# Kernel tuning notes

Hardware: AMD Instinct MI355X
Metric: run time of the kernel (lower is better)

## Reference

```python
import jax, jax.numpy as jnp
import numpy as np

B, L, D_IN, D_MODEL, D_OUT, N_LAYERS, N2 = 16, 2048, 512, 512, 512, 4, 32
Q_STEP = 1.0 / 64.0
LN_EPS = 1e-5


def setup_inputs() -> dict:
    key = jax.random.key(0)
    ks = jax.random.split(key, 12)
    H = D_MODEL
    x = jax.random.normal(ks[0], (B, D_IN, L), jnp.float32)
    # sigma-delta dense encoder / decoder weights (ANN-equivalent: dense + ReLU)
    W_enc = jax.random.normal(ks[1], (H, D_IN), jnp.float32) * (1.0 / np.sqrt(D_IN))
    W_dec = jax.random.normal(ks[2], (D_OUT, H), jnp.float32) * (1.0 / np.sqrt(H))
    # S4D kernel params, stacked over layers. S4D-Lin init.
    log_dt = (jax.random.uniform(ks[3], (N_LAYERS, H), jnp.float32)
              * (np.log(0.1) - np.log(0.001)) + np.log(0.001))
    log_A_real = jnp.full((N_LAYERS, H, N2), np.log(0.5), jnp.float32)
    A_imag = jnp.tile((np.pi * jnp.arange(N2, dtype=jnp.float32))[None, None, :],
                      (N_LAYERS, H, 1))
    C_re = jax.random.normal(ks[4], (N_LAYERS, H, N2), jnp.float32) * (0.5 ** 0.5)
    C_im = jax.random.normal(ks[5], (N_LAYERS, H, N2), jnp.float32) * (0.5 ** 0.5)
    D = jax.random.normal(ks[6], (N_LAYERS, H), jnp.float32)
    # output linear of each S4D block: 1x1 conv H -> 2H followed by GLU
    W_out = jax.random.normal(ks[7], (N_LAYERS, 2 * H, H), jnp.float32) * (1.0 / np.sqrt(H))
    b_out = jnp.zeros((N_LAYERS, 2 * H), jnp.float32)
    ln_g = jnp.ones((N_LAYERS, H), jnp.float32)
    ln_b = jnp.zeros((N_LAYERS, H), jnp.float32)
    return {"x": x, "W_enc": W_enc, "W_dec": W_dec, "log_dt": log_dt,
            "log_A_real": log_A_real, "A_imag": A_imag, "C_re": C_re,
            "C_im": C_im, "D": D, "W_out": W_out, "b_out": b_out,
            "ln_g": ln_g, "ln_b": ln_b}


def _quantize_ste(x, step):
    q = jnp.round(x / step) * step
    return x + jax.lax.stop_gradient(q - x)


def reference(x, W_enc, W_dec, log_dt, log_A_real, A_imag, C_re, C_im, D,
              W_out, b_out, ln_g, ln_b):
    # x: (B, d_input, L) channel-time layout (slayer convention)
    xq = _quantize_ste(x, Q_STEP)
    h = jax.nn.relu(jnp.einsum('bct,dc->bdt', xq, W_enc))  # encoder (B,H,L)
    Lx = h.shape[-1]
    t = jnp.arange(Lx)
    for i in range(N_LAYERS):
        # ---- S4D kernel (ZOH-style discretization) ----
        dt = jnp.exp(log_dt[i])[:, None]                 # (H,1)
        A = -jnp.exp(log_A_real[i]) + 1j * A_imag[i]     # (H,N)
        dtA = dt * A                                     # (H,N)
        Cc = (C_re[i] + 1j * C_im[i]) * jnp.expm1(dtA) / A
        vand = jnp.exp(dtA[:, :, None] * t)              # (H,N,L)
        K = 2.0 * jnp.einsum('hn,hnl->hl', Cc, vand).real  # (H,L)
        # ---- FFT convolution ----
        k_f = jnp.fft.rfft(K, n=2 * Lx)                  # (H, L+1)
        u_f = jnp.fft.rfft(h, n=2 * Lx)                  # (B,H,L+1)
        y = jnp.fft.irfft(u_f * k_f[None], n=2 * Lx)[..., :Lx]
        y = y + D[i][:, None] * h                        # skip connection
        y = jax.nn.gelu(y, approximate=False)
        # output linear: 1x1 conv H->2H + GLU over channel dim
        z = jnp.einsum('bht,dh->bdt', y, W_out[i]) + b_out[i][None, :, None]
        z = z[:, :D_MODEL] * jax.nn.sigmoid(z[:, D_MODEL:])
        # residual + post-norm (LayerNorm over channel dim)
        h = z + h
        mu = h.mean(axis=1, keepdims=True)
        var = h.var(axis=1, keepdims=True)
        h = (h - mu) / jnp.sqrt(var + LN_EPS) * ln_g[i][:, None] + ln_b[i][:, None]
    out = jax.nn.relu(jnp.einsum('bht,dh->bdt', h, W_dec))  # decoder (B,d_out,L)
    return out
```

## Files before the change

### kernel.cpp

```cpp
#include <hip/hip_runtime.h>
#include <cstdint>
#include <cstddef>

typedef __attribute__((ext_vector_type(8))) short short8;
typedef __attribute__((ext_vector_type(8))) _Float16 half8;
typedef __attribute__((ext_vector_type(4))) float floatx4;
typedef __attribute__((ext_vector_type(4))) int intx4;
typedef __attribute__((ext_vector_type(4))) unsigned short ushort4v;

__device__ __forceinline__ unsigned short f2h(float f) {
    union { _Float16 h; unsigned short u; } v;
    v.h = (_Float16)f;
    return v.u;
}
__device__ __forceinline__ float h2f(unsigned short u) {
    union { unsigned short u; _Float16 h; } v;
    v.u = u;
    return (float)v.h;
}
__device__ __forceinline__ float relu_keepnan(float v) {
    return v > 0.f ? v : (v == v ? 0.f : v);
}

__global__ __launch_bounds__(256) void k_cvt(
    const float* __restrict__ src, unsigned short* __restrict__ dst, int n) {
    int i = blockIdx.x * 256 + threadIdx.x;
    if (i < n) dst[i] = f2h(src[i]);
}

__global__ __launch_bounds__(256) void k_precompute(
    const float* __restrict__ ldt, const float* __restrict__ lar,
    const float* __restrict__ aim, const float* __restrict__ cre,
    const float* __restrict__ cim, float4* __restrict__ lwc,
    float2* __restrict__ wt) {
    int idx = blockIdx.x * 256 + threadIdx.x;
    int i = idx >> 14;
    int h = (idx >> 5) & 511;
    int n = idx & 31;
    float dt = expf(ldt[i * 512 + h]);
    float Are = -expf(lar[idx]);
    float Aim = aim[idx];
    float dre = dt * Are, dim = dt * Aim;
    float e = expf(dre);
    float wre = e * cosf(dim);
    float wim = e * sinf(dim);
    float emr = wre - 1.f, emi = wim;
    float inv = 1.f / (Are * Are + Aim * Aim);
    float fr = (emr * Are + emi * Aim) * inv;
    float fi = (emi * Are - emr * Aim) * inv;
    float cr = cre[idx], ci = cim[idx];
    float4 o;
    o.x = wre; o.y = wim;
    o.z = 2.f * (cr * fr - ci * fi);
    o.w = 2.f * (cr * fi + ci * fr);
    int oidx = (i * 32 + n) * 512 + h;
    lwc[oidx] = o;
    float ar = wre, ai = wim;
#pragma unroll
    for (int k = 0; k < 7; ++k) {
        float nr = ar * ar - ai * ai;
        float ni = 2.f * ar * ai;
        ar = nr; ai = ni;
    }
    wt[oidx] = make_float2(ar, ai);
}

__global__ __launch_bounds__(256) void k_quant_transpose(
    const float* __restrict__ x, unsigned short* __restrict__ xq, int b0) {
    __shared__ unsigned short tile[64][65];
    const int bg = b0 + blockIdx.z, bl = blockIdx.z;
    const int c0 = blockIdx.y * 64, t0 = blockIdx.x * 64;
    const int tid = threadIdx.x;
#pragma unroll
    for (int it = 0; it < 16; ++it) {
        int idx = it * 256 + tid;
        int r = idx >> 6, cc = idx & 63;
        float f = x[(size_t)(bg * 512 + c0 + r) * 2048 + t0 + cc];
        float q = rintf(f * 64.f) * 0.015625f;
        tile[r][cc] = f2h(q);
    }
    __syncthreads();
#pragma unroll
    for (int it = 0; it < 16; ++it) {
        int idx = it * 256 + tid;
        int r = idx >> 6, cc = idx & 63;
        xq[(size_t)(bl * 2048 + t0 + r) * 512 + c0 + cc] = tile[cc][r];
    }
}

__global__ __launch_bounds__(64) void k_build_wa(
    const float4* __restrict__ lwc, unsigned short* __restrict__ WA, int layer) {
    __shared__ unsigned short Ws[64 * 136];
    const int h = blockIdx.x, tid = threadIdx.x;
    if (tid < 32) {
        float4 v = lwc[((size_t)layer * 32 + tid) * 512 + h];
        float pr = 1.f, pi = 0.f;
        for (int m = 0; m < 128; ++m) {
            Ws[(2 * tid) * 136 + (127 - m)] = f2h(pr);
            Ws[(2 * tid + 1) * 136 + (127 - m)] = f2h(pi);
            float nr = pr * v.x - pi * v.y;
            float ni = pr * v.y + pi * v.x;
            pr = nr; pi = ni;
        }
    }
    __syncthreads();
#pragma unroll
    for (int it = 0; it < 16; ++it) {
        int idx = it * 64 + tid;
        int r = idx >> 4, c8 = idx & 15;
        *(intx4*)(WA + (size_t)h * 8192 + r * 128 + c8 * 8) =
            *(const intx4*)(Ws + r * 136 + c8 * 8);
    }
}

__global__ __launch_bounds__(256) void k_build_T(
    const float4* __restrict__ lwc, const float* __restrict__ Dp,
    unsigned short* __restrict__ TT, int layer) {
    __shared__ float Kvs[128];
    __shared__ unsigned short Mxs[128 * 64];
    __shared__ float wr_s[32], wi_s[32], cr_s[32], ci_s[32];
    const int h = blockIdx.x, tid = threadIdx.x;
    if (tid < 32) {
        float4 v = lwc[((size_t)layer * 32 + tid) * 512 + h];
        wr_s[tid] = v.x; wi_s[tid] = v.y; cr_s[tid] = v.z; ci_s[tid] = v.w;
    }
    __syncthreads();
    if (tid < 32) {
        const int n = tid;
        float wre = wr_s[n], wim = wi_s[n];
        float ar = cr_s[n], ai = ci_s[n];
        for (int m = 0; m <= 128; ++m) {
            if (m < 128) {
                float s = ar;
#pragma unroll
                for (int d = 16; d >= 1; d >>= 1) s += __shfl_xor(s, d, 64);
                if (n == 0) Kvs[m] = s;
            }
            if (m >= 1) {
                Mxs[(m - 1) * 64 + 2 * n] = f2h(ar);
                Mxs[(m - 1) * 64 + 2 * n + 1] = f2h(-ai);
            }
            float nr = ar * wre - ai * wim;
            float ni = ar * wim + ai * wre;
            ar = nr; ai = ni;
        }
    }
    __syncthreads();
    const float Dh = Dp[layer * 512 + h];
#pragma unroll
    for (int it = 0; it < 12; ++it) {
        int idx = it * 256 + tid;
        int t = idx / 24, c8 = idx % 24;
        short8 pack;
#pragma unroll
        for (int q = 0; q < 8; ++q) {
            int k = c8 * 8 + q;
            unsigned short us;
            if (k < 128) {
                float val = (k <= t) ? (Kvs[t - k] + (k == t ? Dh : 0.f)) : 0.f;
                us = f2h(val);
            } else {
                us = Mxs[t * 64 + (k - 128)];
            }
            pack[q] = (short)us;
        }
        *(short8*)(TT + (size_t)h * 24576 + t * 192 + c8 * 8) = pack;
    }
}

template <int MODE>
__global__ __launch_bounds__(256, 3) void k_gemm(
    const unsigned short* __restrict__ A, const unsigned short* __restrict__ Bm,
    float* __restrict__ of32, unsigned short* __restrict__ o16,
    unsigned short* __restrict__ ut, int J, int b0) {
    __shared__ __align__(16) unsigned short lds[2 * 128 * 72];
    unsigned short* Al = lds;
    unsigned short* Bl = lds + 128 * 72;
    const int tid = threadIdx.x;
    const int m0 = blockIdx.y * 128;
    const int j0 = blockIdx.x * 128;
    const int sub = tid & 7;
    const int row = tid >> 3;
    const unsigned short* Ag = A + (size_t)(m0 + row) * 512 + sub * 8;
    const unsigned short* Bg = Bm + (size_t)(j0 + row) * 512 + sub * 8;
    intx4 ra[4], rb[4];
#pragma unroll
    for (int i = 0; i < 4; ++i) {
        ra[i] = *(const intx4*)(Ag + (size_t)i * 32 * 512);
        rb[i] = *(const intx4*)(Bg + (size_t)i * 32 * 512);
    }
    const int lane = tid & 63;
    const int w = tid >> 6;
    const int wm = w & 1, wn = w >> 1;
    const int l15 = lane & 15, quad = lane >> 4;
    floatx4 acc[4][4] = {};
    for (int kt = 0; kt < 8; ++kt) {
#pragma unroll
        for (int i = 0; i < 4; ++i) {
            *(intx4*)(Al + (row + 32 * i) * 72 + sub * 8) = ra[i];
            *(intx4*)(Bl + (row + 32 * i) * 72 + sub * 8) = rb[i];
        }
        __syncthreads();
        if (kt < 7) {
#pragma unroll
            for (int i = 0; i < 4; ++i) {
                ra[i] = *(const intx4*)(Ag + (size_t)i * 32 * 512 + (kt + 1) * 64);
                rb[i] = *(const intx4*)(Bg + (size_t)i * 32 * 512 + (kt + 1) * 64);
            }
        }
#pragma unroll
        for (int ks = 0; ks < 2; ++ks) {
            half8 af[4], bfr[4];
#pragma unroll
            for (int mt = 0; mt < 4; ++mt)
                af[mt] = *(const half8*)(Al + (wm * 64 + mt * 16 + l15) * 72 + ks * 32 + quad * 8);
#pragma unroll
            for (int nt = 0; nt < 4; ++nt)
                bfr[nt] = *(const half8*)(Bl + (wn * 64 + nt * 16 + l15) * 72 + ks * 32 + quad * 8);
#pragma unroll
            for (int mt = 0; mt < 4; ++mt)
#pragma unroll
                for (int nt = 0; nt < 4; ++nt)
                    acc[mt][nt] = __builtin_amdgcn_mfma_f32_16x16x32_f16(
                        af[mt], bfr[nt], acc[mt][nt], 0, 0, 0);
        }
        __syncthreads();
    }
#pragma unroll
    for (int mt = 0; mt < 4; ++mt) {
#pragma unroll
        for (int nt = 0; nt < 4; ++nt) {
            const int dl = wm * 64 + mt * 16 + quad * 4;
            const int jl = wn * 64 + nt * 16 + l15;
            floatx4 v = acc[mt][nt];
#pragma unroll
            for (int r = 0; r < 4; ++r) v[r] = relu_keepnan(v[r]);
            if (MODE == 0) {
                ushort4v hv;
#pragma unroll
                for (int r = 0; r < 4; ++r) hv[r] = f2h(v[r]);
                *(ushort4v*)(o16 + (size_t)(j0 + jl) * 512 + m0 + dl) = hv;
#pragma unroll
                for (int r = 0; r < 4; ++r) lds[(dl + r) * 136 + jl] = hv[r];
            } else {
                const int j = j0 + jl;
                const int bl = j >> 11, t = j & 2047;
#pragma unroll
                for (int r = 0; r < 4; ++r)
                    of32[((size_t)((b0 + bl) * 512 + m0 + dl + r)) * 2048 + t] = v[r];
            }
        }
    }
    if (MODE == 0) {
        __syncthreads();
        const int drow = tid >> 1, hh = tid & 1;
        const unsigned short* srcp = lds + drow * 136 + hh * 64;
        unsigned short* dstp = ut + (size_t)(m0 + drow) * J + j0 + hh * 64;
#pragma unroll
        for (int q = 0; q < 8; ++q)
            *(intx4*)(dstp + q * 8) = *(const intx4*)(srcp + q * 8);
    }
}

__global__ __launch_bounds__(256, 4) void k_stateA_comb(
    const unsigned short* __restrict__ WA, const unsigned short* __restrict__ ut,
    const float2* __restrict__ wt, unsigned short* __restrict__ S0,
    int layer, int J, int Rtot) {
    __shared__ __align__(16) char smem[64 * 131 * 4];
    unsigned short* Aw = (unsigned short*)smem;
    unsigned short* Bw = (unsigned short*)(smem + 64 * 72 * 2);
    float* Ps = (float*)smem;
    const int tid = threadIdx.x;
    const int h = blockIdx.y;
    const int r0 = blockIdx.x * 128;
    const int sub = tid & 7, row = tid >> 3;
    const unsigned short* Ag = WA + (size_t)h * 8192 + row * 128 + sub * 8;
    const unsigned short* Bg = ut + (size_t)h * J + (size_t)(r0 + row) * 128 + sub * 8;
    intx4 ra[2], rb[4];
    ra[0] = *(const intx4*)(Ag);
    ra[1] = *(const intx4*)(Ag + 32 * 128);
#pragma unroll
    for (int i = 0; i < 4; ++i) rb[i] = *(const intx4*)(Bg + i * 32 * 128);
    const int lane = tid & 63, w = tid >> 6;
    const int wm = w & 1, wn = w >> 1;
    const int l15 = lane & 15, quad = lane >> 4;
    floatx4 acc[2][4] = {};
    for (int kt = 0; kt < 2; ++kt) {
        *(intx4*)(Aw + row * 72 + sub * 8) = ra[0];
        *(intx4*)(Aw + (row + 32) * 72 + sub * 8) = ra[1];
#pragma unroll
        for (int i = 0; i < 4; ++i)
            *(intx4*)(Bw + (row + 32 * i) * 72 + sub * 8) = rb[i];
        __syncthreads();
        if (kt == 0) {
            ra[0] = *(const intx4*)(Ag + 64);
            ra[1] = *(const intx4*)(Ag + 32 * 128 + 64);
#pragma unroll
            for (int i = 0; i < 4; ++i) rb[i] = *(const intx4*)(Bg + i * 32 * 128 + 64);
        }
#pragma unroll
        for (int ks = 0; ks < 2; ++ks) {
            half8 af[2], bfr[4];
#pragma unroll
            for (int mt = 0; mt < 2; ++mt)
                af[mt] = *(const half8*)(Aw + (wm * 32 + mt * 16 + l15) * 72 + ks * 32 + quad * 8);
#pragma unroll
            for (int nt = 0; nt < 4; ++nt)
                bfr[nt] = *(const half8*)(Bw + (wn * 64 + nt * 16 + l15) * 72 + ks * 32 + quad * 8);
#pragma unroll
            for (int mt = 0; mt < 2; ++mt)
#pragma unroll
                for (int nt = 0; nt < 4; ++nt)
                    acc[mt][nt] = __builtin_amdgcn_mfma_f32_16x16x32_f16(
                        af[mt], bfr[nt], acc[mt][nt], 0, 0, 0);
        }
        __syncthreads();
    }
#pragma unroll
    for (int mt = 0; mt < 2; ++mt)
#pragma unroll
        for (int nt = 0; nt < 4; ++nt)
#pragma unroll
            for (int r = 0; r < 4; ++r)
                Ps[(wm * 32 + mt * 16 + quad * 4 + r) * 131 +
                   wn * 64 + nt * 16 + l15] = acc[mt][nt][r];
    __syncthreads();
    const int n = tid & 31, bl = tid >> 5;
    const float2 wv = wt[((size_t)layer * 32 + n) * 512 + h];
    unsigned int* S0w = (unsigned int*)(S0 + ((size_t)h * Rtot + r0 + bl * 16) * 64) + n;
    float ar = 0.f, ai = 0.f;
#pragma unroll
    for (int g = 0; g < 16; ++g) {
        S0w[g * 32] = (unsigned int)f2h(ar) | ((unsigned int)f2h(ai) << 16);
        float pr = Ps[(2 * n) * 131 + bl * 16 + g];
        float pi = Ps[(2 * n + 1) * 131 + bl * 16 + g];
        float nr = fmaf(wv.x, ar, fmaf(-wv.y, ai, pr));
        float ni = fmaf(wv.x, ai, fmaf(wv.y, ar, pi));
        ar = nr; ai = ni;
    }
}

__global__ __launch_bounds__(256, 3) void k_applyB(
    const unsigned short* __restrict__ TT, const unsigned short* __restrict__ ut,
    const unsigned short* __restrict__ S0, unsigned short* __restrict__ vt,
    int J, int Rtot) {
    __shared__ __align__(16) unsigned short lds[2 * 128 * 72];
    unsigned short* Al = lds;
    unsigned short* Bl = lds + 128 * 72;
    const int tid = threadIdx.x;
    const int h = blockIdx.y;
    const int r0 = blockIdx.x * 128;
    const int sub = tid & 7, row = tid >> 3;
    const unsigned short* Ag = TT + (size_t)h * 24576 + row * 192 + sub * 8;
    const unsigned short* Bu = ut + (size_t)h * J + (size_t)(r0 + row) * 128 + sub * 8;
    const unsigned short* Bs = S0 + ((size_t)h * Rtot + r0 + row) * 64 + sub * 8;
    intx4 ra[4], rb[4];
#pragma unroll
    for (int i = 0; i < 4; ++i) {
        ra[i] = *(const intx4*)(Ag + i * 32 * 192);
        rb[i] = *(const intx4*)(Bu + i * 32 * 128);
    }
    const int lane = tid & 63, w = tid >> 6;
    const int wm = w & 1, wn = w >> 1;
    const int l15 = lane & 15, quad = lane >> 4;
    floatx4 acc[4][4] = {};
    for (int kt = 0; kt < 3; ++kt) {
#pragma unroll
        for (int i = 0; i < 4; ++i) {
            *(intx4*)(Al + (row + 32 * i) * 72 + sub * 8) = ra[i];
            *(intx4*)(Bl + (row + 32 * i) * 72 + sub * 8) = rb[i];
        }
        __syncthreads();
        if (kt == 0) {
#pragma unroll
            for (int i = 0; i < 4; ++i) {
                ra[i] = *(const intx4*)(Ag + i * 32 * 192 + 64);
                rb[i] = *(const intx4*)(Bu + i * 32 * 128 + 64);
            }
        } else if (kt == 1) {
#pragma unroll
            for (int i = 0; i < 4; ++i) {
                ra[i] = *(const intx4*)(Ag + i * 32 * 192 + 128);
                rb[i] = *(const intx4*)(Bs + i * 32 * 64);
            }
        }
#pragma unroll
        for (int ks = 0; ks < 2; ++ks) {
            half8 af[4], bfr[4];
#pragma unroll
            for (int mt = 0; mt < 4; ++mt)
                af[mt] = *(const half8*)(Al + (wm * 64 + mt * 16 + l15) * 72 + ks * 32 + quad * 8);
#pragma unroll
            for (int nt = 0; nt < 4; ++nt)
                bfr[nt] = *(const half8*)(Bl + (wn * 64 + nt * 16 + l15) * 72 + ks * 32 + quad * 8);
#pragma unroll
            for (int mt = 0; mt < 4; ++mt)
#pragma unroll
                for (int nt = 0; nt < 4; ++nt)
                    acc[mt][nt] = __builtin_amdgcn_mfma_f32_16x16x32_f16(
                        af[mt], bfr[nt], acc[mt][nt], 0, 0, 0);
        }
        __syncthreads();
    }
#pragma unroll
    for (int mt = 0; mt < 4; ++mt)
#pragma unroll
        for (int nt = 0; nt < 4; ++nt) {
            const int tl = wm * 64 + mt * 16 + quad * 4;
            const int rl = wn * 64 + nt * 16 + l15;
            ushort4v pack;
#pragma unroll
            for (int r = 0; r < 4; ++r) {
                float y = acc[mt][nt][r];
                float ge = 0.5f * y * (1.f + erff(y * 0.70710678118654752f));
                pack[r] = f2h(ge);
            }
            *(ushort4v*)(lds + rl * 136 + tl) = pack;
        }
    __syncthreads();
    const int rl2 = tid >> 1, hh = tid & 1;
    const unsigned short* srcp = lds + rl2 * 136 + hh * 64;
    unsigned short* dstp = vt + (size_t)h * J + (size_t)(r0 + rl2) * 128 + hh * 64;
#pragma unroll
    for (int q = 0; q < 8; ++q)
        *(intx4*)(dstp + q * 8) = *(const intx4*)(srcp + q * 8);
}

__global__ __launch_bounds__(256, 2) void k_gemm_glu(
    const unsigned short* __restrict__ A,
    const unsigned short* __restrict__ Bt,
    const float* __restrict__ bias,
    unsigned short* __restrict__ g_out, int J) {
    __shared__ __align__(16) unsigned short lds[3 * 128 * 72];
    unsigned short* A1l = lds;
    unsigned short* A2l = lds + 9216;
    unsigned short* Bl  = lds + 18432;
    const int tid = threadIdx.x;
    const int m0 = blockIdx.y * 128;
    const int j0 = blockIdx.x * 128;
    const int sub = tid & 7;
    const int row = tid >> 3;
    const unsigned short* A1g = A + (size_t)(m0 + row) * 512 + sub * 8;
    const unsigned short* A2g = A1g + 512 * 512;
    const int chp = tid >> 3, jo = tid & 7;
    const unsigned short* Bg = Bt + (size_t)(2 * chp) * J + j0 + jo * 8;
    intx4 ra1[4], ra2[4], rb[4];
#pragma unroll
    for (int i = 0; i < 4; ++i) {
        ra1[i] = *(const intx4*)(A1g + (size_t)i * 32 * 512);
        ra2[i] = *(const intx4*)(A2g + (size_t)i * 32 * 512);
    }
    rb[0] = *(const intx4*)(Bg);
    rb[1] = *(const intx4*)(Bg + J);
    rb[2] = *(const intx4*)(Bg + 64);
    rb[3] = *(const intx4*)(Bg + J + 64);
    const int lane = tid & 63;
    const int w = tid >> 6;
    const int wm = w & 1, wn = w >> 1;
    const int l15 = lane & 15, quad = lane >> 4;
    const int colbase = (((chp >> 2) ^ jo) << 3) + (chp & 3) * 2;
    floatx4 ac1[4][4] = {}, ac2[4][4] = {};
    for (int kt = 0; kt < 8; ++kt) {
#pragma unroll
        for (int i = 0; i < 4; ++i) {
            *(intx4*)(A1l + (row + 32 * i) * 72 + sub * 8) = ra1[i];
            *(intx4*)(A2l + (row + 32 * i) * 72 + sub * 8) = ra2[i];
        }
        {
            unsigned int* B32 = (unsigned int*)Bl;
#pragma unroll
            for (int half = 0; half < 2; ++half) {
                const int jb = (jo + half * 8) * 8;
                intx4 e0 = rb[half * 2], e1 = rb[half * 2 + 1];
#pragma unroll
                for (int i = 0; i < 4; ++i) {
                    unsigned int ae = (unsigned int)e0[i], be = (unsigned int)e1[i];
                    unsigned int lo = (ae & 0xffffu) | (be << 16);
                    unsigned int hi = (ae >> 16) | (be & 0xffff0000u);
                    B32[((jb + 2 * i) * 72 + colbase) >> 1] = lo;
                    B32[((jb + 2 * i + 1) * 72 + colbase) >> 1] = hi;
                }
            }
        }
        __syncthreads();
        if (kt < 7) {
#pragma unroll
            for (int i = 0; i < 4; ++i) {
                ra1[i] = *(const intx4*)(A1g + (size_t)i * 32 * 512 + (kt + 1) * 64);
                ra2[i] = *(const intx4*)(A2g + (size_t)i * 32 * 512 + (kt + 1) * 64);
            }
            rb[0] = *(const intx4*)(Bg + (size_t)(kt + 1) * 64 * J);
            rb[1] = *(const intx4*)(Bg + (size_t)(kt + 1) * 64 * J + J);
            rb[2] = *(const intx4*)(Bg + (size_t)(kt + 1) * 64 * J + 64);
            rb[3] = *(const intx4*)(Bg + (size_t)(kt + 1) * 64 * J + J + 64);
        }
#pragma unroll
        for (int ks = 0; ks < 2; ++ks) {
            half8 af1[4], af2[4], bfr[4];
#pragma unroll
            for (int mt = 0; mt < 4; ++mt) {
                af1[mt] = *(const half8*)(A1l + (wm * 64 + mt * 16 + l15) * 72 + ks * 32 + quad * 8);
                af2[mt] = *(const half8*)(A2l + (wm * 64 + mt * 16 + l15) * 72 + ks * 32 + quad * 8);
            }
#pragma unroll
            for (int nt = 0; nt < 4; ++nt) {
                const int rr = wn * 64 + nt * 16 + l15;
                const int cb = (ks * 4 + quad) ^ ((rr >> 3) & 7);
                bfr[nt] = *(const half8*)(Bl + rr * 72 + cb * 8);
            }
#pragma unroll
            for (int mt = 0; mt < 4; ++mt)
#pragma unroll
                for (int nt = 0; nt < 4; ++nt) {
                    ac1[mt][nt] = __builtin_amdgcn_mfma_f32_16x16x32_f16(
                        af1[mt], bfr[nt], ac1[mt][nt], 0, 0, 0);
                    ac2[mt][nt] = __builtin_amdgcn_mfma_f32_16x16x32_f16(
                        af2[mt], bfr[nt], ac2[mt][nt], 0, 0, 0);
                }
        }
        __syncthreads();
    }
#pragma unroll
    for (int mt = 0; mt < 4; ++mt) {
#pragma unroll
        for (int nt = 0; nt < 4; ++nt) {
            const int dl = wm * 64 + mt * 16 + quad * 4;
            const int jl = wn * 64 + nt * 16 + l15;
            ushort4v p;
#pragma unroll
            for (int r = 0; r < 4; ++r) {
                float a = ac1[mt][nt][r] + bias[m0 + dl + r];
                float gg = ac2[mt][nt][r] + bias[512 + m0 + dl + r];
                p[r] = f2h(a / (1.f + expf(-gg)));
            }
            *(ushort4v*)(lds + jl * 136 + dl) = p;
        }
    }
    __syncthreads();
    const int r2 = tid >> 1, hh = tid & 1;
    const unsigned short* srcp = lds + r2 * 136 + hh * 64;
    unsigned short* dstp = g_out + (size_t)(j0 + r2) * 512 + m0 + hh * 64;
#pragma unroll
    for (int q = 0; q < 8; ++q)
        *(intx4*)(dstp + q * 8) = *(const intx4*)(srcp + q * 8);
}

__global__ __launch_bounds__(256, 4) void k_res_ln_t(
    const unsigned short* __restrict__ g, unsigned short* __restrict__ hf,
    unsigned short* __restrict__ ut, unsigned short* __restrict__ hb,
    const float* __restrict__ lng, const float* __restrict__ lnb,
    int layer, int J, int mode) {
    __shared__ unsigned short tile[64 * 40];
    const int tid = threadIdx.x;
    const int r = tid >> 3, sub = tid & 7;
    const int j0 = blockIdx.x * 32;
    const size_t j = (size_t)j0 + r;
    const unsigned short* gj = g + j * 512;
    unsigned short* hj = hf + j * 512;
    floatx4 v[16];
    float s1 = 0.f, s2 = 0.f;
#pragma unroll
    for (int k = 0; k < 16; ++k) {
        ushort4v gv = *(const ushort4v*)(gj + sub * 4 + k * 32);
        ushort4v hv = *(const ushort4v*)(hj + sub * 4 + k * 32);
        floatx4 vv;
#pragma unroll
        for (int i = 0; i < 4; ++i) vv[i] = h2f(gv[i]) + h2f(hv[i]);
        v[k] = vv;
        s1 += vv[0] + vv[1] + vv[2] + vv[3];
        s2 += vv[0] * vv[0] + vv[1] * vv[1] + vv[2] * vv[2] + vv[3] * vv[3];
    }
#pragma unroll
    for (int m = 4; m >= 1; m >>= 1) { s1 += __shfl_xor(s1, m, 64); s2 += __shfl_xor(s2, m, 64); }
    const float mu = s1 * (1.f / 512.f);
    const float var = s2 * (1.f / 512.f) - mu * mu;
    const float isd = 1.f / sqrtf(var + 1e-5f);
#pragma unroll
    for (int t = 0; t < 8; ++t) {
        if (mode == 1 && t) __syncthreads();
#pragma unroll
        for (int kk = 0; kk < 2; ++kk) {
            const int k = t * 2 + kk;
            const int cho = sub * 4 + k * 32;
            floatx4 gw = *(const floatx4*)(lng + layer * 512 + cho);
            floatx4 bw = *(const floatx4*)(lnb + layer * 512 + cho);
            ushort4v p;
#pragma unroll
            for (int i = 0; i < 4; ++i)
                p[i] = f2h((v[k][i] - mu) * isd * gw[i] + bw[i]);
            if (mode == 1) {
                *(ushort4v*)(hj + cho) = p;
                const int chl = kk * 32 + sub * 4;
#pragma unroll
                for (int i = 0; i < 4; ++i)
                    tile[(chl + i) * 40 + (r ^ ((((chl + i) >> 2) & 3) << 3))] = p[i];
            } else {
                *(ushort4v*)(hb + j * 512 + cho) = p;
            }
        }
        if (mode == 1) {
            __syncthreads();
            const int chrow = tid >> 2, part = tid & 3;
            const int pb = part ^ ((chrow >> 2) & 3);
            *(intx4*)(ut + (size_t)(t * 64 + chrow) * J + j0 + part * 8) =
                *(const intx4*)(tile + chrow * 40 + pb * 8);
        }
    }
}

extern "C" void kernel_launch(void* const* d_in, const int* in_sizes, int n_in,
                              void* d_out, int out_size, void* d_ws, size_t ws_size,
                              hipStream_t stream) {
    (void)in_sizes; (void)n_in; (void)out_size;
    const float* x      = (const float*)d_in[0];
    const float* W_enc  = (const float*)d_in[1];
    const float* W_dec  = (const float*)d_in[2];
    const float* log_dt = (const float*)d_in[3];
    const float* log_Ar = (const float*)d_in[4];
    const float* A_im   = (const float*)d_in[5];
    const float* C_re   = (const float*)d_in[6];
    const float* C_im   = (const float*)d_in[7];
    const float* Dp     = (const float*)d_in[8];
    const float* W_out  = (const float*)d_in[9];
    const float* b_out  = (const float*)d_in[10];
    const float* ln_g   = (const float*)d_in[11];
    const float* ln_b   = (const float*)d_in[12];

    int C = 16;
    while (C > 8 && (size_t)C * (9ull << 20) + (42ull << 20) > ws_size) C >>= 1;
    const size_t J = (size_t)C * 2048;
    const int Rtot = C * 16;

    char* ws = (char*)d_ws;
    size_t off = 0;
    auto alloc = [&](size_t bytes) { void* p = ws + off; off += (bytes + 255) & ~(size_t)255; return p; };
    float4*         lwc   = (float4*)alloc(4ull * 512 * 32 * 16);
    float2*         wt    = (float2*)alloc(4ull * 512 * 32 * 8);
    unsigned short* wencb = (unsigned short*)alloc(512 * 512 * 2);
    unsigned short* wdecb = (unsigned short*)alloc(512 * 512 * 2);
    unsigned short* woutb = (unsigned short*)alloc(4ull * 1024 * 512 * 2);
    unsigned short* WAb   = (unsigned short*)alloc(512ull * 64 * 128 * 2);
    unsigned short* TTb   = (unsigned short*)alloc(512ull * 128 * 192 * 2);
    unsigned short* ut    = (unsigned short*)alloc(512ull * J * 2);
    char*           scan  = (char*)alloc((size_t)C * (3ull << 20));
    unsigned short* hf    = (unsigned short*)alloc(J * 512 * 2);
    unsigned short* vt    = (unsigned short*)alloc(J * 512 * 2);
    unsigned short* g16   = (unsigned short*)scan;
    unsigned short* xq    = (unsigned short*)scan;
    unsigned short* hb    = vt;
    unsigned short* S0u   = (unsigned short*)(scan + (size_t)C * (2ull << 20));

    k_precompute<<<256, 256, 0, stream>>>(log_dt, log_Ar, A_im, C_re, C_im, lwc, wt);
    k_cvt<<<1024, 256, 0, stream>>>(W_enc, wencb, 512 * 512);
    k_cvt<<<1024, 256, 0, stream>>>(W_dec, wdecb, 512 * 512);
    k_cvt<<<8192, 256, 0, stream>>>(W_out, woutb, 4 * 1024 * 512);
    for (int b0 = 0; b0 < 16; b0 += C) {
        k_quant_transpose<<<dim3(32, 8, C), 256, 0, stream>>>(x, xq, b0);
        k_gemm<0><<<dim3(C * 16, 4), 256, 0, stream>>>(wencb, xq, nullptr, hf, ut, (int)J, 0);
        for (int i = 0; i < 4; ++i) {
            k_build_wa<<<512, 64, 0, stream>>>(lwc, WAb, i);
            k_build_T<<<512, 256, 0, stream>>>(lwc, Dp, TTb, i);
            k_stateA_comb<<<dim3(Rtot / 128, 512), 256, 0, stream>>>(
                WAb, ut, wt, S0u, i, (int)J, Rtot);
            k_applyB<<<dim3(Rtot / 128, 512), 256, 0, stream>>>(TTb, ut, S0u, vt, (int)J, Rtot);
            k_gemm_glu<<<dim3(C * 16, 4), 256, 0, stream>>>(
                woutb + (size_t)i * 1024 * 512, vt, b_out + (size_t)i * 1024, g16, (int)J);
            k_res_ln_t<<<(int)(J / 32), 256, 0, stream>>>(
                g16, hf, ut, hb, ln_g, ln_b, i, (int)J, (i == 3) ? 2 : 1);
        }
        k_gemm<2><<<dim3(C * 16, 4), 256, 0, stream>>>(wdecb, hb, (float*)d_out, nullptr, nullptr, (int)J, b0);
    }
}
```

Measured before the change: 874.0 us.

## Fuse chunk-state computation and apply step into one S4D kernel via LDS

Merges the state-accumulation kernel and the apply kernel into a single kernel per (chunk block, channel), so the per-chunk initial states stay in LDS instead of being written to and reread from a global scratch buffer. This removes one launch per layer and the S0 global round trip. The ut tile is loaded from global twice within the block instead of once per kernel. Separately, the GLU GEMM's A-tile LDS row stride shrinks from 72 to 68 halves and its launch bound rises to 3 blocks per CU, aiming for higher occupancy at some risk of bank conflicts.

```diff
diff --git a/kernel.cpp b/kernel.cpp
--- a/kernel.cpp
+++ b/kernel.cpp
@@ -262,179 +262,180 @@
     }
 }
 
-__global__ __launch_bounds__(256, 4) void k_stateA_comb(
-    const unsigned short* __restrict__ WA, const unsigned short* __restrict__ ut,
-    const float2* __restrict__ wt, unsigned short* __restrict__ S0,
-    int layer, int J, int Rtot) {
-    __shared__ __align__(16) char smem[64 * 131 * 4];
-    unsigned short* Aw = (unsigned short*)smem;
-    unsigned short* Bw = (unsigned short*)(smem + 64 * 72 * 2);
-    float* Ps = (float*)smem;
+__global__ __launch_bounds__(256, 3) void k_s4d_fused(
+    const unsigned short* __restrict__ WA,
+    const unsigned short* __restrict__ TT,
+    const unsigned short* __restrict__ ut,
+    const float2* __restrict__ wt,
+    unsigned short* __restrict__ vt,
+    int layer, int J) {
+    __shared__ __align__(16) char smem[54272];
+    unsigned short* Aw  = (unsigned short*)smem;
+    unsigned short* Bw  = (unsigned short*)(smem + 9216);
+    float*          Ps  = (float*)smem;
+    unsigned short* Al  = (unsigned short*)smem;
+    unsigned short* Bl  = (unsigned short*)(smem + 18432);
+    unsigned short* S0l = (unsigned short*)(smem + 36864);
+    unsigned short* til = (unsigned short*)smem;
     const int tid = threadIdx.x;
     const int h = blockIdx.y;
     const int r0 = blockIdx.x * 128;
     const int sub = tid & 7, row = tid >> 3;
-    const unsigned short* Ag = WA + (size_t)h * 8192 + row * 128 + sub * 8;
-    const unsigned short* Bg = ut + (size_t)h * J + (size_t)(r0 + row) * 128 + sub * 8;
-    intx4 ra[2], rb[4];
-    ra[0] = *(const intx4*)(Ag);
-    ra[1] = *(const intx4*)(Ag + 32 * 128);
-#pragma unroll
-    for (int i = 0; i < 4; ++i) rb[i] = *(const intx4*)(Bg + i * 32 * 128);
     const int lane = tid & 63, w = tid >> 6;
     const int wm = w & 1, wn = w >> 1;
     const int l15 = lane & 15, quad = lane >> 4;
-    floatx4 acc[2][4] = {};
-    for (int kt = 0; kt < 2; ++kt) {
-        *(intx4*)(Aw + row * 72 + sub * 8) = ra[0];
-        *(intx4*)(Aw + (row + 32) * 72 + sub * 8) = ra[1];
-#pragma unroll
-        for (int i = 0; i < 4; ++i)
-            *(intx4*)(Bw + (row + 32 * i) * 72 + sub * 8) = rb[i];
-        __syncthreads();
-        if (kt == 0) {
-            ra[0] = *(const intx4*)(Ag + 64);
-            ra[1] = *(const intx4*)(Ag + 32 * 128 + 64);
-#pragma unroll
-            for (int i = 0; i < 4; ++i) rb[i] = *(const intx4*)(Bg + i * 32 * 128 + 64);
-        }
-#pragma unroll
-        for (int ks = 0; ks < 2; ++ks) {
-            half8 af[2], bfr[4];
-#pragma unroll
-            for (int mt = 0; mt < 2; ++mt)
-                af[mt] = *(const half8*)(Aw + (wm * 32 + mt * 16 + l15) * 72 + ks * 32 + quad * 8);
+    const unsigned short* Bgu = ut + (size_t)h * J + (size_t)(r0 + row) * 128 + sub * 8;
+    {
+        const unsigned short* Ag = WA + (size_t)h * 8192 + row * 128 + sub * 8;
+        intx4 ra[2], rb[4];
+        ra[0] = *(const intx4*)(Ag);
+        ra[1] = *(const intx4*)(Ag + 32 * 128);
+#pragma unroll
+        for (int i = 0; i < 4; ++i) rb[i] = *(const intx4*)(Bgu + i * 32 * 128);
+        floatx4 acc[2][4] = {};
+        for (int kt = 0; kt < 2; ++kt) {
+            *(intx4*)(Aw + row * 72 + sub * 8) = ra[0];
+            *(intx4*)(Aw + (row + 32) * 72 + sub * 8) = ra[1];
+#pragma unroll
+            for (int i = 0; i < 4; ++i)
+                *(intx4*)(Bw + (row + 32 * i) * 72 + sub * 8) = rb[i];
+            __syncthreads();
+            if (kt == 0) {
+                ra[0] = *(const intx4*)(Ag + 64);
+                ra[1] = *(const intx4*)(Ag + 32 * 128 + 64);
+#pragma unroll
+                for (int i = 0; i < 4; ++i) rb[i] = *(const intx4*)(Bgu + i * 32 * 128 + 64);
+            }
+#pragma unroll
+            for (int ks = 0; ks < 2; ++ks) {
+                half8 af[2], bfr[4];
+#pragma unroll
+                for (int mt = 0; mt < 2; ++mt)
+                    af[mt] = *(const half8*)(Aw + (wm * 32 + mt * 16 + l15) * 72 + ks * 32 + quad * 8);
+#pragma unroll
+                for (int nt = 0; nt < 4; ++nt)
+                    bfr[nt] = *(const half8*)(Bw + (wn * 64 + nt * 16 + l15) * 72 + ks * 32 + quad * 8);
+#pragma unroll
+                for (int mt = 0; mt < 2; ++mt)
+#pragma unroll
+                    for (int nt = 0; nt < 4; ++nt)
+                        acc[mt][nt] = __builtin_amdgcn_mfma_f32_16x16x32_f16(
+                            af[mt], bfr[nt], acc[mt][nt], 0, 0, 0);
+            }
+            __syncthreads();
+        }
+#pragma unroll
+        for (int mt = 0; mt < 2; ++mt)
 #pragma unroll
             for (int nt = 0; nt < 4; ++nt)
-                bfr[nt] = *(const half8*)(Bw + (wn * 64 + nt * 16 + l15) * 72 + ks * 32 + quad * 8);
-#pragma unroll
-            for (int mt = 0; mt < 2; ++mt)
-#pragma unroll
-                for (int nt = 0; nt < 4; ++nt)
-                    acc[mt][nt] = __builtin_amdgcn_mfma_f32_16x16x32_f16(
-                        af[mt], bfr[nt], acc[mt][nt], 0, 0, 0);
-        }
-        __syncthreads();
-    }
-#pragma unroll
-    for (int mt = 0; mt < 2; ++mt)
-#pragma unroll
-        for (int nt = 0; nt < 4; ++nt)
-#pragma unroll
-            for (int r = 0; r < 4; ++r)
-                Ps[(wm * 32 + mt * 16 + quad * 4 + r) * 131 +
-                   wn * 64 + nt * 16 + l15] = acc[mt][nt][r];
-    __syncthreads();
-    const int n = tid & 31, bl = tid >> 5;
-    const float2 wv = wt[((size_t)layer * 32 + n) * 512 + h];
-    unsigned int* S0w = (unsigned int*)(S0 + ((size_t)h * Rtot + r0 + bl * 16) * 64) + n;
-    float ar = 0.f, ai = 0.f;
-#pragma unroll
-    for (int g = 0; g < 16; ++g) {
-        S0w[g * 32] = (unsigned int)f2h(ar) | ((unsigned int)f2h(ai) << 16);
-        float pr = Ps[(2 * n) * 131 + bl * 16 + g];
-        float pi = Ps[(2 * n + 1) * 131 + bl * 16 + g];
-        float nr = fmaf(wv.x, ar, fmaf(-wv.y, ai, pr));
-        float ni = fmaf(wv.x, ai, fmaf(wv.y, ar, pi));
-        ar = nr; ai = ni;
-    }
-}
-
-__global__ __launch_bounds__(256, 3) void k_applyB(
-    const unsigned short* __restrict__ TT, const unsigned short* __restrict__ ut,
-    const unsigned short* __restrict__ S0, unsigned short* __restrict__ vt,
-    int J, int Rtot) {
-    __shared__ __align__(16) unsigned short lds[2 * 128 * 72];
-    unsigned short* Al = lds;
-    unsigned short* Bl = lds + 128 * 72;
-    const int tid = threadIdx.x;
-    const int h = blockIdx.y;
-    const int r0 = blockIdx.x * 128;
-    const int sub = tid & 7, row = tid >> 3;
-    const unsigned short* Ag = TT + (size_t)h * 24576 + row * 192 + sub * 8;
-    const unsigned short* Bu = ut + (size_t)h * J + (size_t)(r0 + row) * 128 + sub * 8;
-    const unsigned short* Bs = S0 + ((size_t)h * Rtot + r0 + row) * 64 + sub * 8;
-    intx4 ra[4], rb[4];
-#pragma unroll
-    for (int i = 0; i < 4; ++i) {
-        ra[i] = *(const intx4*)(Ag + i * 32 * 192);
-        rb[i] = *(const intx4*)(Bu + i * 32 * 128);
-    }
-    const int lane = tid & 63, w = tid >> 6;
-    const int wm = w & 1, wn = w >> 1;
-    const int l15 = lane & 15, quad = lane >> 4;
-    floatx4 acc[4][4] = {};
-    for (int kt = 0; kt < 3; ++kt) {
+#pragma unroll
+                for (int r = 0; r < 4; ++r)
+                    Ps[(wm * 32 + mt * 16 + quad * 4 + r) * 131 +
+                       wn * 64 + nt * 16 + l15] = acc[mt][nt][r];
+        __syncthreads();
+    }
+    {
+        const int n = tid & 31, blx = tid >> 5;
+        const float2 wv = wt[((size_t)layer * 32 + n) * 512 + h];
+        unsigned int* S32 = (unsigned int*)S0l;
+        float ar = 0.f, ai = 0.f;
+#pragma unroll
+        for (int g = 0; g < 16; ++g) {
+            S32[(blx * 16 + g) * 34 + n] = (unsigned int)f2h(ar) | ((unsigned int)f2h(ai) << 16);
+            float pr = Ps[(2 * n) * 131 + blx * 16 + g];
+            float pi = Ps[(2 * n + 1) * 131 + blx * 16 + g];
+            float nr = fmaf(wv.x, ar, fmaf(-wv.y, ai, pr));
+            float ni = fmaf(wv.x, ai, fmaf(wv.y, ar, pi));
+            ar = nr; ai = ni;
+        }
+        __syncthreads();
+    }
+    {
+        const unsigned short* Ag = TT + (size_t)h * 24576 + row * 192 + sub * 8;
+        intx4 ra[4], rb[4];
 #pragma unroll
         for (int i = 0; i < 4; ++i) {
-            *(intx4*)(Al + (row + 32 * i) * 72 + sub * 8) = ra[i];
-            *(intx4*)(Bl + (row + 32 * i) * 72 + sub * 8) = rb[i];
-        }
-        __syncthreads();
-        if (kt == 0) {
-#pragma unroll
-            for (int i = 0; i < 4; ++i) {
-                ra[i] = *(const intx4*)(Ag + i * 32 * 192 + 64);
-                rb[i] = *(const intx4*)(Bu + i * 32 * 128 + 64);
-            }
-        } else if (kt == 1) {
-#pragma unroll
-            for (int i = 0; i < 4; ++i) {
-                ra[i] = *(const intx4*)(Ag + i * 32 * 192 + 128);
-                rb[i] = *(const intx4*)(Bs + i * 32 * 64);
-            }
-        }
-#pragma unroll
-        for (int ks = 0; ks < 2; ++ks) {
-            half8 af[4], bfr[4];
-#pragma unroll
-            for (int mt = 0; mt < 4; ++mt)
-                af[mt] = *(const half8*)(Al + (wm * 64 + mt * 16 + l15) * 72 + ks * 32 + quad * 8);
-#pragma unroll
-            for (int nt = 0; nt < 4; ++nt)
-                bfr[nt] = *(const half8*)(Bl + (wn * 64 + nt * 16 + l15) * 72 + ks * 32 + quad * 8);
-#pragma unroll
-            for (int mt = 0; mt < 4; ++mt)
-#pragma unroll
-                for (int nt = 0; nt < 4; ++nt)
-                    acc[mt][nt] = __builtin_amdgcn_mfma_f32_16x16x32_f16(
-                        af[mt], bfr[nt], acc[mt][nt], 0, 0, 0);
-        }
-        __syncthreads();
-    }
-#pragma unroll
-    for (int mt = 0; mt < 4; ++mt)
-#pragma unroll
-        for (int nt = 0; nt < 4; ++nt) {
-            const int tl = wm * 64 + mt * 16 + quad * 4;
-            const int rl = wn * 64 + nt * 16 + l15;
-            ushort4v pack;
-#pragma unroll
-            for (int r = 0; r < 4; ++r) {
-                float y = acc[mt][nt][r];
-                float ge = 0.5f * y * (1.f + erff(y * 0.70710678118654752f));
-                pack[r] = f2h(ge);
-            }
-            *(ushort4v*)(lds + rl * 136 + tl) = pack;
-        }
-    __syncthreads();
-    const int rl2 = tid >> 1, hh = tid & 1;
-    const unsigned short* srcp = lds + rl2 * 136 + hh * 64;
-    unsigned short* dstp = vt + (size_t)h * J + (size_t)(r0 + rl2) * 128 + hh * 64;
-#pragma unroll
-    for (int q = 0; q < 8; ++q)
-        *(intx4*)(dstp + q * 8) = *(const intx4*)(srcp + q * 8);
-}
-
-__global__ __launch_bounds__(256, 2) void k_gemm_glu(
+            ra[i] = *(const intx4*)(Ag + i * 32 * 192);
+            rb[i] = *(const intx4*)(Bgu + i * 32 * 128);
+        }
+        floatx4 acc[4][4] = {};
+        for (int kt = 0; kt < 3; ++kt) {
+#pragma unroll
+            for (int i = 0; i < 4; ++i)
+                *(intx4*)(Al + (row + 32 * i) * 72 + sub * 8) = ra[i];
+            if (kt < 2) {
+#pragma unroll
+                for (int i = 0; i < 4; ++i)
+                    *(intx4*)(Bl + (row + 32 * i) * 72 + sub * 8) = rb[i];
+            }
+            __syncthreads();
+            if (kt == 0) {
+#pragma unroll
+                for (int i = 0; i < 4; ++i) {
+                    ra[i] = *(const intx4*)(Ag + i * 32 * 192 + 64);
+                    rb[i] = *(const intx4*)(Bgu + i * 32 * 128 + 64);
+                }
+            } else if (kt == 1) {
+#pragma unroll
+                for (int i = 0; i < 4; ++i)
+                    ra[i] = *(const intx4*)(Ag + i * 32 * 192 + 128);
+            }
+#pragma unroll
+            for (int ks = 0; ks < 2; ++ks) {
+                half8 af[4], bfr[4];
+#pragma unroll
+                for (int mt = 0; mt < 4; ++mt)
+                    af[mt] = *(const half8*)(Al + (wm * 64 + mt * 16 + l15) * 72 + ks * 32 + quad * 8);
+#pragma unroll
+                for (int nt = 0; nt < 4; ++nt) {
+                    const int rr = wn * 64 + nt * 16 + l15;
+                    bfr[nt] = (kt < 2)
+                        ? *(const half8*)(Bl + rr * 72 + ks * 32 + quad * 8)
+                        : *(const half8*)(S0l + rr * 68 + ks * 32 + quad * 8);
+                }
+#pragma unroll
+                for (int mt = 0; mt < 4; ++mt)
+#pragma unroll
+                    for (int nt = 0; nt < 4; ++nt)
+                        acc[mt][nt] = __builtin_amdgcn_mfma_f32_16x16x32_f16(
+                            af[mt], bfr[nt], acc[mt][nt], 0, 0, 0);
+            }
+            __syncthreads();
+        }
+#pragma unroll
+        for (int mt = 0; mt < 4; ++mt)
+#pragma unroll
+            for (int nt = 0; nt < 4; ++nt) {
+                const int tl = wm * 64 + mt * 16 + quad * 4;
+                const int rl = wn * 64 + nt * 16 + l15;
+                ushort4v pack;
+#pragma unroll
+                for (int r = 0; r < 4; ++r) {
+                    float y = acc[mt][nt][r];
+                    float ge = 0.5f * y * (1.f + erff(y * 0.70710678118654752f));
+                    pack[r] = f2h(ge);
+                }
+                *(ushort4v*)(til + rl * 136 + tl) = pack;
+            }
+        __syncthreads();
+        const int rl2 = tid >> 1, hh = tid & 1;
+        const unsigned short* srcp = til + rl2 * 136 + hh * 64;
+        unsigned short* dstp = vt + (size_t)h * J + (size_t)(r0 + rl2) * 128 + hh * 64;
+#pragma unroll
+        for (int q = 0; q < 8; ++q)
+            *(intx4*)(dstp + q * 8) = *(const intx4*)(srcp + q * 8);
+    }
+}
+
+__global__ __launch_bounds__(256, 3) void k_gemm_glu(
     const unsigned short* __restrict__ A,
     const unsigned short* __restrict__ Bt,
     const float* __restrict__ bias,
     unsigned short* __restrict__ g_out, int J) {
-    __shared__ __align__(16) unsigned short lds[3 * 128 * 72];
+    __shared__ __align__(16) unsigned short lds[26624];
     unsigned short* A1l = lds;
-    unsigned short* A2l = lds + 9216;
-    unsigned short* Bl  = lds + 18432;
+    unsigned short* A2l = lds + 8704;
+    unsigned short* Bl  = lds + 17408;
     const int tid = threadIdx.x;
     const int m0 = blockIdx.y * 128;
     const int j0 = blockIdx.x * 128;
@@ -463,8 +464,8 @@
     for (int kt = 0; kt < 8; ++kt) {
 #pragma unroll
         for (int i = 0; i < 4; ++i) {
-            *(intx4*)(A1l + (row + 32 * i) * 72 + sub * 8) = ra1[i];
-            *(intx4*)(A2l + (row + 32 * i) * 72 + sub * 8) = ra2[i];
+            *(intx4*)(A1l + (row + 32 * i) * 68 + sub * 8) = ra1[i];
+            *(intx4*)(A2l + (row + 32 * i) * 68 + sub * 8) = ra2[i];
         }
         {
             unsigned int* B32 = (unsigned int*)Bl;
@@ -499,8 +500,8 @@
             half8 af1[4], af2[4], bfr[4];
 #pragma unroll
             for (int mt = 0; mt < 4; ++mt) {
-                af1[mt] = *(const half8*)(A1l + (wm * 64 + mt * 16 + l15) * 72 + ks * 32 + quad * 8);
-                af2[mt] = *(const half8*)(A2l + (wm * 64 + mt * 16 + l15) * 72 + ks * 32 + quad * 8);
+                af1[mt] = *(const half8*)(A1l + (wm * 64 + mt * 16 + l15) * 68 + ks * 32 + quad * 8);
+                af2[mt] = *(const half8*)(A2l + (wm * 64 + mt * 16 + l15) * 68 + ks * 32 + quad * 8);
             }
 #pragma unroll
             for (int nt = 0; nt < 4; ++nt) {
@@ -648,7 +649,6 @@
     unsigned short* g16   = (unsigned short*)scan;
     unsigned short* xq    = (unsigned short*)scan;
     unsigned short* hb    = vt;
-    unsigned short* S0u   = (unsigned short*)(scan + (size_t)C * (2ull << 20));
 
     k_precompute<<<256, 256, 0, stream>>>(log_dt, log_Ar, A_im, C_re, C_im, lwc, wt);
     k_cvt<<<1024, 256, 0, stream>>>(W_enc, wencb, 512 * 512);
@@ -660,9 +660,8 @@
         for (int i = 0; i < 4; ++i) {
             k_build_wa<<<512, 64, 0, stream>>>(lwc, WAb, i);
             k_build_T<<<512, 256, 0, stream>>>(lwc, Dp, TTb, i);
-            k_stateA_comb<<<dim3(Rtot / 128, 512), 256, 0, stream>>>(
-                WAb, ut, wt, S0u, i, (int)J, Rtot);
-            k_applyB<<<dim3(Rtot / 128, 512), 256, 0, stream>>>(TTb, ut, S0u, vt, (int)J, Rtot);
+            k_s4d_fused<<<dim3(Rtot / 128, 512), 256, 0, stream>>>(
+                WAb, TTb, ut, wt, vt, i, (int)J);
             k_gemm_glu<<<dim3(C * 16, 4), 256, 0, stream>>>(
                 woutb + (size_t)i * 1024 * 512, vt, b_out + (size_t)i * 1024, g16, (int)J);
             k_res_ln_t<<<(int)(J / 32), 256, 0, stream>>>(
```

After: 1.328 ms. +52.0%, slower.
